# Optimization experiments

Hardware: AMD Instinct MI355X
Metric: run time of the kernel (lower is better)

## Reference

```python
import jax, jax.numpy as jnp
import numpy as np

HID = 128

def _gru_states(x, w_ih, w_hh, b_ih, b_hh):
    # x: [B,T,I]; w_ih: [3H,I]; w_hh: [3H,H]; biases: [3H]
    # Precompute input projections for all timesteps (one big GEMM).
    gi = jnp.einsum('bti,gi->tbg', x, w_ih) + b_ih  # [T,B,3H]
    B = x.shape[0]
    h0 = jnp.zeros((B, HID), dtype=x.dtype)

    def step(h, gi_t):
        gh = h @ w_hh.T + b_hh                      # [B,3H]
        i_r, i_z, i_n = jnp.split(gi_t, 3, axis=-1)
        h_r, h_z, h_n = jnp.split(gh, 3, axis=-1)
        r = jax.nn.sigmoid(i_r + h_r)
        z = jax.nn.sigmoid(i_z + h_z)
        n = jnp.tanh(i_n + r * h_n)
        h_new = (1.0 - z) * n + z * h
        return h_new, h_new

    _, states = jax.lax.scan(step, h0, gi)          # states: [T,B,H]
    return states


def setup_inputs() -> dict:
    key = jax.random.key(0)
    ks = jax.random.split(key, 7)
    B, T, I, H, E = 64, 2048, 128, HID, 64
    s_ih = 1.0 / np.sqrt(I)
    s_hh = 1.0 / np.sqrt(H)
    s_p = 1.0 / np.sqrt(H)
    return {
        'x': jax.random.normal(ks[0], (B, T, I), dtype=jnp.float32),
        'w_ih': jax.random.uniform(ks[1], (3 * H, I), jnp.float32, -s_ih, s_ih),
        'w_hh': jax.random.uniform(ks[2], (3 * H, H), jnp.float32, -s_hh, s_hh),
        'b_ih': jax.random.uniform(ks[3], (3 * H,), jnp.float32, -s_hh, s_hh),
        'b_hh': jax.random.uniform(ks[4], (3 * H,), jnp.float32, -s_hh, s_hh),
        'w_proj': jax.random.uniform(ks[5], (E, H), jnp.float32, -s_p, s_p),
        'b_proj': jax.random.uniform(ks[6], (E,), jnp.float32, -s_p, s_p),
    }


def reference(x, w_ih, w_hh, b_ih, b_hh, w_proj, b_proj):
    states = _gru_states(x, w_ih, w_hh, b_ih, b_hh)  # [T,B,H]
    pooled = states.mean(axis=0)                     # mean pooling over time -> [B,H]
    return pooled @ w_proj.T + b_proj                # [B,E]
```

## Files before the change

### kernel.cpp

```cpp
#include <hip/hip_runtime.h>
#include <math.h>

#define B_   64
#define T_   2048
#define HID_ 128
#define G3_  384
#define IN_  128
#define E_   64

#define TS_  128

typedef _Float16 h2f  __attribute__((ext_vector_type(2)));
typedef _Float16 f16x8 __attribute__((ext_vector_type(8)));
typedef float    f32x4 __attribute__((ext_vector_type(4)));

__device__ __forceinline__ float rcp_(float x)     { return __builtin_amdgcn_rcpf(x); }
__device__ __forceinline__ float sigmoid_(float x) { return rcp_(1.f + __expf(-x)); }
__device__ __forceinline__ float tanh_(float x)    { return 1.f - 2.f * rcp_(1.f + __expf(2.f * x)); }

__device__ __forceinline__ f16x8 pack8_(float4 a, float4 b) {
    uint4 u;
    u.x = __builtin_bit_cast(unsigned, __builtin_amdgcn_cvt_pkrtz(a.x, a.y));
    u.y = __builtin_bit_cast(unsigned, __builtin_amdgcn_cvt_pkrtz(a.z, a.w));
    u.z = __builtin_bit_cast(unsigned, __builtin_amdgcn_cvt_pkrtz(b.x, b.y));
    u.w = __builtin_bit_cast(unsigned, __builtin_amdgcn_cvt_pkrtz(b.z, b.w));
    return __builtin_bit_cast(f16x8, u);
}

__global__ __launch_bounds__(256, 1)
void gi_gemm(const float* __restrict__ x, const float* __restrict__ w_ih,
             const float* __restrict__ b_ih, const float* __restrict__ b_hh,
             float* __restrict__ gi, int t0)
{
    const int tid = threadIdx.x;
    const int w   = tid >> 6;
    const int l   = tid & 63;
    const int ln  = l & 15;
    const int kq  = l >> 4;
    const int tt  = blockIdx.x;
    const int b   = blockIdx.y;
    const int tl_base = tt * TS_ + w * 32;

    float bias_r[24];
    #pragma unroll
    for (int nt = 0; nt < 24; nt++) {
        const int col = nt * 16 + ln;
        bias_r[nt] = b_ih[col] + (col < 256 ? b_hh[col] : 0.f);
    }

    f32x4 acc[2][24];
    #pragma unroll
    for (int mt = 0; mt < 2; mt++)
        #pragma unroll
        for (int nt = 0; nt < 24; nt++)
            acc[mt][nt] = (f32x4){0.f, 0.f, 0.f, 0.f};

    const float* xb = x + ((size_t)b * T_ + (size_t)(t0 + tl_base)) * IN_;

    #pragma unroll
    for (int kc = 0; kc < 4; kc++) {
        const int ko = kc * 32 + kq * 8;
        f16x8 afr[2];
        #pragma unroll
        for (int mt = 0; mt < 2; mt++) {
            const float* xr = xb + (size_t)(mt * 16 + ln) * IN_ + ko;
            float4 p0 = *reinterpret_cast<const float4*>(xr);
            float4 p1 = *reinterpret_cast<const float4*>(xr + 4);
            afr[mt] = pack8_(p0, p1);
        }
        #pragma unroll
        for (int nt = 0; nt < 24; nt++) {
            const float* wr = w_ih + (size_t)(nt * 16 + ln) * IN_ + ko;
            float4 q0 = *reinterpret_cast<const float4*>(wr);
            float4 q1 = *reinterpret_cast<const float4*>(wr + 4);
            const f16x8 bfr = pack8_(q0, q1);
            acc[0][nt] = __builtin_amdgcn_mfma_f32_16x16x32_f16(afr[0], bfr, acc[0][nt], 0, 0, 0);
            acc[1][nt] = __builtin_amdgcn_mfma_f32_16x16x32_f16(afr[1], bfr, acc[1][nt], 0, 0, 0);
        }
    }

    #pragma unroll
    for (int mt = 0; mt < 2; mt++) {
        #pragma unroll
        for (int r = 0; r < 4; r++) {
            const size_t trow = (size_t)(tl_base + mt * 16 + kq * 4 + r);
            float* go = gi + trow * (B_ * G3_) + (size_t)b * G3_ + ln;
            #pragma unroll
            for (int nt = 0; nt < 24; nt++)
                go[nt * 16] = acc[mt][nt][r] + bias_r[nt];
        }
    }
}

#define REC_STEP(CUR, LD, TLOAD, PB)                                           \
  {                                                                            \
    const float* gp_ = gib + (size_t)(TLOAD) * S;                              \
    LD[0] = gp_[c0];       LD[1] = gp_[c0 + 64];                               \
    LD[2] = gp_[c0 + 128]; LD[3] = gp_[c0 + 192];                              \
    LD[4] = gp_[c0 + 256]; LD[5] = gp_[c0 + 320];                              \
    const char* hb_ = (const char*)(&h2_sh[PB][0]) + kq * 16;                  \
    f16x8 af_[4];                                                              \
    af_[0] = __builtin_bit_cast(f16x8, *(const uint4*)(hb_));                  \
    af_[1] = __builtin_bit_cast(f16x8, *(const uint4*)(hb_ + 64));             \
    af_[2] = __builtin_bit_cast(f16x8, *(const uint4*)(hb_ + 128));            \
    af_[3] = __builtin_bit_cast(f16x8, *(const uint4*)(hb_ + 192));            \
    f32x4 ac_[6];                                                              \
    _Pragma("unroll")                                                          \
    for (int m = 0; m < 6; m++) ac_[m] = (f32x4){0.f, 0.f, 0.f, 0.f};          \
    _Pragma("unroll")                                                          \
    for (int kc = 0; kc < 4; kc++) {                                           \
      _Pragma("unroll")                                                        \
      for (int m = 0; m < 6; m++)                                              \
        ac_[m] = __builtin_amdgcn_mfma_f32_16x16x32_f16(af_[kc], wfr[m][kc],   \
                                                        ac_[m], 0, 0, 0);      \
    }                                                                          \
    const float r0 = sigmoid_(CUR[0] + ac_[0][0]);                             \
    const float r1 = sigmoid_(CUR[1] + ac_[1][0]);                             \
    const float z0 = sigmoid_(CUR[2] + ac_[2][0]);                             \
    const float z1 = sigmoid_(CUR[3] + ac_[3][0]);                             \
    const float n0 = tanh_(CUR[4] + r0 * (ac_[4][0] + bh0));                   \
    const float n1 = tanh_(CUR[5] + r1 * (ac_[5][0] + bh1));                   \
    hj0 = (1.f - z0) * n0 + z0 * hj0;                                          \
    hj1 = (1.f - z1) * n1 + z1 * hj1;                                          \
    hs0 += hj0; hs1 += hj1;                                                    \
    if (kq == 0) {                                                             \
      h2_sh[(PB) ^ 1][c0] = (_Float16)hj0;                                     \
      h2_sh[(PB) ^ 1][c1] = (_Float16)hj1;                                     \
    }                                                                          \
    __syncthreads();                                                           \
  }

__global__ __launch_bounds__(256, 1)
void rec_kernel(const float* __restrict__ gi, const float* __restrict__ w_hh,
                const float* __restrict__ b_hh,
                const float* __restrict__ w_proj, const float* __restrict__ b_proj,
                float* __restrict__ out, float* __restrict__ state,
                int t0, int t1)
{
    const int tid  = threadIdx.x;
    const int b    = blockIdx.x;
    const int w    = tid >> 6;
    const int lane = tid & 63;
    const int ln   = lane & 15;
    const int kq   = lane >> 4;
    const int c0   = 16 * w + ln;
    const int c1   = c0 + 64;
    const int nT   = t1 - t0;

    __shared__ _Float16 h2_sh[2][HID_];
    __shared__ float pooled[HID_];

    f16x8 wfr[6][4];
    #pragma unroll
    for (int m = 0; m < 6; m++) {
        const float* wr = w_hh + (size_t)(c0 + 64 * m) * HID_;
        #pragma unroll
        for (int kc = 0; kc < 4; kc++) {
            const float* p = wr + kc * 32 + kq * 8;
            float4 q0 = *reinterpret_cast<const float4*>(p);
            float4 q1 = *reinterpret_cast<const float4*>(p + 4);
            wfr[m][kc] = pack8_(q0, q1);
        }
    }
    const float bh0 = b_hh[256 + c0];
    const float bh1 = b_hh[256 + c1];

    float hj0, hj1, hs0, hs1;
    if (t0 == 0) { hj0 = hj1 = hs0 = hs1 = 0.f; }
    else {
        hj0 = state[b * HID_ + c0];             hj1 = state[b * HID_ + c1];
        hs0 = state[B_ * HID_ + b * HID_ + c0]; hs1 = state[B_ * HID_ + b * HID_ + c1];
    }
    if (kq == 0) {
        h2_sh[0][c0] = (_Float16)hj0;
        h2_sh[0][c1] = (_Float16)hj1;
    }
    __syncthreads();

    const float* gib = gi + (size_t)b * G3_;
    const size_t S = (size_t)B_ * G3_;

    float g0[6], g1[6], g2[6], g3[6];
    {
        const float* p0 = gib;
        const float* p1 = gib + S;
        g0[0]=p0[c0]; g0[1]=p0[c0+64]; g0[2]=p0[c0+128]; g0[3]=p0[c0+192]; g0[4]=p0[c0+256]; g0[5]=p0[c0+320];
        g1[0]=p1[c0]; g1[1]=p1[c0+64]; g1[2]=p1[c0+128]; g1[3]=p1[c0+192]; g1[4]=p1[c0+256]; g1[5]=p1[c0+320];
    }

    int pb = 0;
    for (int t = 0; t < nT; t += 4) {
        const int nTm1 = nT - 1;
        int t2 = t + 2 < nTm1 ? t + 2 : nTm1;
        int t3 = t + 3 < nTm1 ? t + 3 : nTm1;
        int t4 = t + 4 < nTm1 ? t + 4 : nTm1;
        int t5 = t + 5 < nTm1 ? t + 5 : nTm1;
        REC_STEP(g0, g2, t2, pb); pb ^= 1;
        REC_STEP(g1, g3, t3, pb); pb ^= 1;
        REC_STEP(g2, g0, t4, pb); pb ^= 1;
        REC_STEP(g3, g1, t5, pb); pb ^= 1;
    }

    if (t1 < T_) {
        if (kq == 0) {
            state[b * HID_ + c0]             = hj0;  state[b * HID_ + c1]             = hj1;
            state[B_ * HID_ + b * HID_ + c0] = hs0;  state[B_ * HID_ + b * HID_ + c1] = hs1;
        }
    } else {
        if (kq == 0) {
            pooled[c0] = hs0 * (1.f / (float)T_);
            pooled[c1] = hs1 * (1.f / (float)T_);
        }
        __syncthreads();
        if (tid < E_) {
            const float4* wpj = reinterpret_cast<const float4*>(w_proj + (size_t)tid * HID_);
            const float4* pp  = reinterpret_cast<const float4*>(pooled);
            float a0 = 0.f, a1 = 0.f, a2 = 0.f, a3 = 0.f;
            #pragma unroll
            for (int k = 0; k < 32; k++) {
                float4 wv = wpj[k]; float4 pv = pp[k];
                a0 = fmaf(wv.x, pv.x, a0);
                a1 = fmaf(wv.y, pv.y, a1);
                a2 = fmaf(wv.z, pv.z, a2);
                a3 = fmaf(wv.w, pv.w, a3);
            }
            out[b * E_ + tid] = (a0 + a1) + (a2 + a3) + b_proj[tid];
        }
    }
}

extern "C" void kernel_launch(void* const* d_in, const int* in_sizes, int n_in,
                              void* d_out, int out_size, void* d_ws, size_t ws_size,
                              hipStream_t stream)
{
    const float* x      = (const float*)d_in[0];
    const float* w_ih   = (const float*)d_in[1];
    const float* w_hh   = (const float*)d_in[2];
    const float* b_ih   = (const float*)d_in[3];
    const float* b_hh   = (const float*)d_in[4];
    const float* w_proj = (const float*)d_in[5];
    const float* b_proj = (const float*)d_in[6];
    float* out = (float*)d_out;

    const size_t state_bytes = (size_t)2 * B_ * HID_ * sizeof(float);
    const size_t per_t = (size_t)B_ * G3_ * sizeof(float);
    size_t avail = ws_size > state_bytes ? ws_size - state_bytes : 0;
    int chunkT = (int)(avail / per_t);
    if (chunkT > T_) chunkT = T_;
    chunkT &= ~(TS_ - 1);
    if (chunkT < TS_) chunkT = TS_;

    float* gi_buf = (float*)d_ws;
    float* state  = (float*)((char*)d_ws + (size_t)chunkT * per_t);

    for (int t0 = 0; t0 < T_; t0 += chunkT) {
        int t1 = t0 + chunkT; if (t1 > T_) t1 = T_;
        int nT = t1 - t0;
        gi_gemm<<<dim3(nT / TS_, B_), dim3(256), 0, stream>>>(x, w_ih, b_ih, b_hh, gi_buf, t0);
        rec_kernel<<<dim3(B_), dim3(256), 0, stream>>>(gi_buf, w_hh, b_hh, w_proj, b_proj,
                                                       out, state, t0, t1);
    }
}
```

Before: 985.5 us.

## Split GRU recurrence across 8 waves and fold log2e into weights

The recurrent kernel now launches 512 threads per batch row instead of 256, so each thread owns one hidden unit. That halves the MFMA chain (3 gates instead of 6) and the gate math per thread on the serial time-step path. The recurrent weights and the n-gate bias are pre-scaled by log2(e) or 2·log2(e), so the sigmoid and tanh evaluations feed exp2 directly without an extra multiply. The cost is a per-step barrier across 8 waves instead of 4, and slightly different fp16 rounding of the scaled weights.

```diff
diff --git a/kernel.cpp b/kernel.cpp
--- a/kernel.cpp
+++ b/kernel.cpp
@@ -13,6 +13,15 @@
 typedef _Float16 h2f  __attribute__((ext_vector_type(2)));
 typedef _Float16 f16x8 __attribute__((ext_vector_type(8)));
 typedef float    f32x4 __attribute__((ext_vector_type(4)));
+
+#define L2E  1.4426950408889634f
+#define L2E2 2.8853900817779268f
+
+#if __has_builtin(__builtin_amdgcn_exp2f)
+#define EXP2(x) __builtin_amdgcn_exp2f(x)
+#else
+#define EXP2(x) __expf((x) * 0.6931471805599453f)
+#endif
 
 __device__ __forceinline__ float rcp_(float x)     { return __builtin_amdgcn_rcpf(x); }
 __device__ __forceinline__ float sigmoid_(float x) { return rcp_(1.f + __expf(-x)); }
@@ -95,42 +104,38 @@
 #define REC_STEP(CUR, LD, TLOAD, PB)                                           \
   {                                                                            \
     const float* gp_ = gib + (size_t)(TLOAD) * S;                              \
-    LD[0] = gp_[c0];       LD[1] = gp_[c0 + 64];                               \
-    LD[2] = gp_[c0 + 128]; LD[3] = gp_[c0 + 192];                              \
-    LD[4] = gp_[c0 + 256]; LD[5] = gp_[c0 + 320];                              \
+    LD[0] = gp_[cg]; LD[1] = gp_[cg + 128]; LD[2] = gp_[cg + 256];             \
     const char* hb_ = (const char*)(&h2_sh[PB][0]) + kq * 16;                  \
     f16x8 af_[4];                                                              \
     af_[0] = __builtin_bit_cast(f16x8, *(const uint4*)(hb_));                  \
     af_[1] = __builtin_bit_cast(f16x8, *(const uint4*)(hb_ + 64));             \
     af_[2] = __builtin_bit_cast(f16x8, *(const uint4*)(hb_ + 128));            \
     af_[3] = __builtin_bit_cast(f16x8, *(const uint4*)(hb_ + 192));            \
-    f32x4 ac_[6];                                                              \
+    f32x4 ac_[3];                                                              \
     _Pragma("unroll")                                                          \
-    for (int m = 0; m < 6; m++) ac_[m] = (f32x4){0.f, 0.f, 0.f, 0.f};          \
+    for (int g = 0; g < 3; g++) ac_[g] = (f32x4){0.f, 0.f, 0.f, 0.f};          \
     _Pragma("unroll")                                                          \
     for (int kc = 0; kc < 4; kc++) {                                           \
       _Pragma("unroll")                                                        \
-      for (int m = 0; m < 6; m++)                                              \
-        ac_[m] = __builtin_amdgcn_mfma_f32_16x16x32_f16(af_[kc], wfr[m][kc],   \
-                                                        ac_[m], 0, 0, 0);      \
+      for (int g = 0; g < 3; g++)                                              \
+        ac_[g] = __builtin_amdgcn_mfma_f32_16x16x32_f16(af_[kc], wf[g][kc],    \
+                                                        ac_[g], 0, 0, 0);      \
     }                                                                          \
-    const float r0 = sigmoid_(CUR[0] + ac_[0][0]);                             \
-    const float r1 = sigmoid_(CUR[1] + ac_[1][0]);                             \
-    const float z0 = sigmoid_(CUR[2] + ac_[2][0]);                             \
-    const float z1 = sigmoid_(CUR[3] + ac_[3][0]);                             \
-    const float n0 = tanh_(CUR[4] + r0 * (ac_[4][0] + bh0));                   \
-    const float n1 = tanh_(CUR[5] + r1 * (ac_[5][0] + bh1));                   \
-    hj0 = (1.f - z0) * n0 + z0 * hj0;                                          \
-    hj1 = (1.f - z1) * n1 + z1 * hj1;                                          \
-    hs0 += hj0; hs1 += hj1;                                                    \
-    if (kq == 0) {                                                             \
-      h2_sh[(PB) ^ 1][c0] = (_Float16)hj0;                                     \
-      h2_sh[(PB) ^ 1][c1] = (_Float16)hj1;                                     \
-    }                                                                          \
+    const float q_  = CUR[2] * L2E2;                                           \
+    const float yr_ = fmaf(CUR[0], L2E, ac_[0][0]);                            \
+    const float r_  = rcp_(1.f + EXP2(-yr_));                                  \
+    const float yz_ = fmaf(CUR[1], L2E, ac_[1][0]);                            \
+    const float z_  = rcp_(1.f + EXP2(-yz_));                                  \
+    const float yn_ = fmaf(r_, ac_[2][0] + bh, q_);                            \
+    const float u_  = rcp_(1.f + EXP2(yn_));                                   \
+    const float n_  = fmaf(-2.f, u_, 1.f);                                     \
+    hj = n_ + z_ * (hj - n_);                                                  \
+    hs += hj;                                                                  \
+    if (kq == 0) h2_sh[(PB) ^ 1][cg] = (_Float16)hj;                           \
     __syncthreads();                                                           \
   }
 
-__global__ __launch_bounds__(256, 1)
+__global__ __launch_bounds__(512, 2)
 void rec_kernel(const float* __restrict__ gi, const float* __restrict__ w_hh,
                 const float* __restrict__ b_hh,
                 const float* __restrict__ w_proj, const float* __restrict__ b_proj,
@@ -143,49 +148,49 @@
     const int lane = tid & 63;
     const int ln   = lane & 15;
     const int kq   = lane >> 4;
-    const int c0   = 16 * w + ln;
-    const int c1   = c0 + 64;
+    const int wh   = w & 3;
+    const int f    = w >> 2;
+    const int cg   = 16 * wh + ln + 64 * f;
     const int nT   = t1 - t0;
 
     __shared__ _Float16 h2_sh[2][HID_];
     __shared__ float pooled[HID_];
 
-    f16x8 wfr[6][4];
-    #pragma unroll
-    for (int m = 0; m < 6; m++) {
-        const float* wr = w_hh + (size_t)(c0 + 64 * m) * HID_;
+    f16x8 wf[3][4];
+    #pragma unroll
+    for (int g = 0; g < 3; g++) {
+        const float s = (g == 2) ? L2E2 : L2E;
+        const float* wr = w_hh + (size_t)(128 * g + cg) * HID_;
         #pragma unroll
         for (int kc = 0; kc < 4; kc++) {
             const float* p = wr + kc * 32 + kq * 8;
             float4 q0 = *reinterpret_cast<const float4*>(p);
             float4 q1 = *reinterpret_cast<const float4*>(p + 4);
-            wfr[m][kc] = pack8_(q0, q1);
-        }
-    }
-    const float bh0 = b_hh[256 + c0];
-    const float bh1 = b_hh[256 + c1];
-
-    float hj0, hj1, hs0, hs1;
-    if (t0 == 0) { hj0 = hj1 = hs0 = hs1 = 0.f; }
+            q0.x *= s; q0.y *= s; q0.z *= s; q0.w *= s;
+            q1.x *= s; q1.y *= s; q1.z *= s; q1.w *= s;
+            wf[g][kc] = pack8_(q0, q1);
+        }
+    }
+    const float bh = L2E2 * b_hh[256 + cg];
+
+    float hj, hs;
+    if (t0 == 0) { hj = hs = 0.f; }
     else {
-        hj0 = state[b * HID_ + c0];             hj1 = state[b * HID_ + c1];
-        hs0 = state[B_ * HID_ + b * HID_ + c0]; hs1 = state[B_ * HID_ + b * HID_ + c1];
-    }
-    if (kq == 0) {
-        h2_sh[0][c0] = (_Float16)hj0;
-        h2_sh[0][c1] = (_Float16)hj1;
-    }
+        hj = state[b * HID_ + cg];
+        hs = state[B_ * HID_ + b * HID_ + cg];
+    }
+    if (kq == 0) h2_sh[0][cg] = (_Float16)hj;
     __syncthreads();
 
     const float* gib = gi + (size_t)b * G3_;
     const size_t S = (size_t)B_ * G3_;
 
-    float g0[6], g1[6], g2[6], g3[6];
+    float g0[3], g1[3], g2[3], g3[3];
     {
         const float* p0 = gib;
         const float* p1 = gib + S;
-        g0[0]=p0[c0]; g0[1]=p0[c0+64]; g0[2]=p0[c0+128]; g0[3]=p0[c0+192]; g0[4]=p0[c0+256]; g0[5]=p0[c0+320];
-        g1[0]=p1[c0]; g1[1]=p1[c0+64]; g1[2]=p1[c0+128]; g1[3]=p1[c0+192]; g1[4]=p1[c0+256]; g1[5]=p1[c0+320];
+        g0[0] = p0[cg]; g0[1] = p0[cg + 128]; g0[2] = p0[cg + 256];
+        g1[0] = p1[cg]; g1[1] = p1[cg + 128]; g1[2] = p1[cg + 256];
     }
 
     int pb = 0;
@@ -203,14 +208,11 @@
 
     if (t1 < T_) {
         if (kq == 0) {
-            state[b * HID_ + c0]             = hj0;  state[b * HID_ + c1]             = hj1;
-            state[B_ * HID_ + b * HID_ + c0] = hs0;  state[B_ * HID_ + b * HID_ + c1] = hs1;
+            state[b * HID_ + cg]             = hj;
+            state[B_ * HID_ + b * HID_ + cg] = hs;
         }
     } else {
-        if (kq == 0) {
-            pooled[c0] = hs0 * (1.f / (float)T_);
-            pooled[c1] = hs1 * (1.f / (float)T_);
-        }
+        if (kq == 0) pooled[cg] = hs * (1.f / (float)T_);
         __syncthreads();
         if (tid < E_) {
             const float4* wpj = reinterpret_cast<const float4*>(w_proj + (size_t)tid * HID_);
@@ -257,7 +259,7 @@
         int t1 = t0 + chunkT; if (t1 > T_) t1 = T_;
         int nT = t1 - t0;
         gi_gemm<<<dim3(nT / TS_, B_), dim3(256), 0, stream>>>(x, w_ih, b_ih, b_hh, gi_buf, t0);
-        rec_kernel<<<dim3(B_), dim3(256), 0, stream>>>(gi_buf, w_hh, b_hh, w_proj, b_proj,
+        rec_kernel<<<dim3(B_), dim3(512), 0, stream>>>(gi_buf, w_hh, b_hh, w_proj, b_proj,
                                                        out, state, t0, t1);
     }
 }
```

Result: faster. 848.5 us (-13.9%).
